# Kernel optimization log

Hardware: AMD Instinct MI355X
Metric: run time of the kernel (lower is better)

Reference implementation:

```python
import jax, jax.numpy as jnp
import numpy as np

N_NODES = 100000
N_EDGES = 1600000


def gcn_conv(x, edge_index, W, b):
    """PyG-style GCNConv: self-loops + symmetric normalization + scatter-add."""
    n = x.shape[0]
    src, dst = edge_index[0], edge_index[1]
    loop = jnp.arange(n, dtype=src.dtype)
    src = jnp.concatenate([src, loop])
    dst = jnp.concatenate([dst, loop])
    h = x @ W  # [n, out] transform before propagate (PyG order)
    deg = jax.ops.segment_sum(jnp.ones_like(dst, dtype=h.dtype), dst, num_segments=n)
    dinv = jnp.where(deg > 0, deg ** -0.5, 0.0)
    norm = dinv[src] * dinv[dst]  # [E+n]
    msgs = h[src] * norm[:, None]  # gather + scale (largest intermediate)
    out = jax.ops.segment_sum(msgs, dst, num_segments=n)
    return out + b


def setup_inputs() -> dict:
    key = jax.random.key(0)
    ks = jax.random.split(key, 8)
    edge_attr = jax.random.normal(ks[0], (N_NODES, 5), dtype=jnp.float32)
    edge_index = jax.random.randint(ks[1], (2, N_EDGES), 0, N_NODES, dtype=jnp.int64)
    def lin(k, fan_in, fan_out):
        bound = 1.0 / np.sqrt(fan_in)
        return jax.random.uniform(k, (fan_in, fan_out), jnp.float32, -bound, bound)
    return {
        "edge_attr": edge_attr,
        "edge_index": edge_index,
        "W1": lin(ks[2], 5, 64),
        "b1": jnp.zeros((64,), jnp.float32),
        "W2": lin(ks[3], 64, 32),
        "b2": jnp.zeros((32,), jnp.float32),
        "fcW1": lin(ks[4], 32, 16),
        "fcb1": jnp.zeros((16,), jnp.float32),
        "fcW2": lin(ks[5], 16, 2),
        "fcb2": jnp.zeros((2,), jnp.float32),
    }


def reference(edge_attr, edge_index, W1, b1, W2, b2, fcW1, fcb1, fcW2, fcb2):
    x = jax.nn.relu(gcn_conv(edge_attr, edge_index, W1, b1))
    x = jax.nn.relu(gcn_conv(x, edge_index, W2, b2))
    x = jax.nn.relu(x @ fcW1 + fcb1)
    return x @ fcW2 + fcb2
```

## Files before the change

### kernel.cpp

```cpp
#include <hip/hip_runtime.h>


#define MS_TILE 2048
#define MAXB 512
#define AGG_NODES 32
#define AGG_STAGE 1024

__global__ __launch_bounds__(256) void histA(const int* __restrict__ dst,
                                             int* __restrict__ histG, int E) {
    __shared__ int h[MAXB];
    int t = threadIdx.x;
    h[t] = 0;
    h[t + 256] = 0;
    __syncthreads();
    int base = blockIdx.x * MS_TILE;
    int cnt = min(MS_TILE, E - base);
    for (int k = t; k < cnt; k += 256) atomicAdd(&h[dst[base + k] >> 8], 1);
    __syncthreads();
    histG[blockIdx.x * MAXB + t] = h[t];
    histG[blockIdx.x * MAXB + 256 + t] = h[t + 256];
}

__global__ __launch_bounds__(256) void scanTiles(const int* __restrict__ histG,
                                                 int* __restrict__ offsG,
                                                 int* __restrict__ bucketTotal,
                                                 int nTiles) {
    __shared__ int scn[256];
    int b = blockIdx.x, t = threadIdx.x;
    int run = 0;
    for (int base = 0; base < nTiles; base += 256) {
        int idx = base + t;
        int v = (idx < nTiles) ? histG[idx * MAXB + b] : 0;
        scn[t] = v;
        __syncthreads();
        int incl = v;
        for (int d = 1; d < 256; d <<= 1) {
            int add = (t >= d) ? scn[t - d] : 0;
            __syncthreads();
            incl += add;
            scn[t] = incl;
            __syncthreads();
        }
        if (idx < nTiles) offsG[idx * MAXB + b] = incl - v + run;
        run += scn[255];
        __syncthreads();
    }
    if (t == 0) bucketTotal[b] = run;
}

__global__ __launch_bounds__(256) void scanBase(const int* __restrict__ bucketTotal,
                                                int* __restrict__ gbase, int E) {
    __shared__ int scn[256];
    int t = threadIdx.x;
    int a0 = bucketTotal[2 * t], a1 = bucketTotal[2 * t + 1];
    int s = a0 + a1;
    scn[t] = s;
    __syncthreads();
    int incl = s;
    for (int d = 1; d < 256; d <<= 1) {
        int add = (t >= d) ? scn[t - d] : 0;
        __syncthreads();
        incl += add;
        scn[t] = incl;
        __syncthreads();
    }
    int ex = incl - s;
    gbase[2 * t] = ex;
    gbase[2 * t + 1] = ex + a0;
    if (t == 255) gbase[MAXB] = E;
}

__global__ __launch_bounds__(256) void multisplit2(
    const int* __restrict__ src, const int* __restrict__ dst,
    const int* __restrict__ histG, const int* __restrict__ offsG,
    const int* __restrict__ gbase, unsigned* __restrict__ binned, int E) {
    __shared__ unsigned stage[MS_TILE];
    __shared__ unsigned short sb[MS_TILE];
    __shared__ int hoff[MAXB + 1];
    __shared__ int hcur[MAXB];
    __shared__ int gb[MAXB];
    __shared__ int scn[256];
    int t = threadIdx.x;
    int tile = blockIdx.x;
    int base = tile * MS_TILE;
    int cnt = min(MS_TILE, E - base);

    int a0 = histG[tile * MAXB + 2 * t];
    int a1 = histG[tile * MAXB + 2 * t + 1];
    gb[2 * t] = gbase[2 * t] + offsG[tile * MAXB + 2 * t];
    gb[2 * t + 1] = gbase[2 * t + 1] + offsG[tile * MAXB + 2 * t + 1];
    int s = a0 + a1;
    scn[t] = s;
    __syncthreads();
    int incl = s;
    for (int d = 1; d < 256; d <<= 1) {
        int add = (t >= d) ? scn[t - d] : 0;
        __syncthreads();
        incl += add;
        scn[t] = incl;
        __syncthreads();
    }
    int ex = incl - s;
    hoff[2 * t] = ex;
    hoff[2 * t + 1] = ex + a0;
    hcur[2 * t] = ex;
    hcur[2 * t + 1] = ex + a0;
    if (t == 255) hoff[MAXB] = cnt;
    __syncthreads();
    for (int k = t; k < cnt; k += 256) {
        int d = dst[base + k];
        int b = d >> 8;
        int p = atomicAdd(&hcur[b], 1);
        stage[p] = ((unsigned)src[base + k] << 8) | (unsigned)(d & 255);
        sb[p] = (unsigned short)b;
    }
    __syncthreads();
    for (int k = t; k < cnt; k += 256) {
        int b = sb[k];
        binned[gb[b] + (k - hoff[b])] = stage[k];
    }
}

__global__ __launch_bounds__(256) void place_fine2(
    const unsigned* __restrict__ binned, const int* __restrict__ gbase,
    const float* __restrict__ x, int* __restrict__ offs, int* __restrict__ deg,
    float* __restrict__ dinv, float* __restrict__ y, int* __restrict__ srcs, int n) {
    __shared__ int cnt[256];
    __shared__ int scn[256];
    __shared__ int lcur[256];
    int t = threadIdx.x, b = blockIdx.x;
    int node0 = b << 8;
    int nn = min(256, n - node0);
    int e0 = gbase[b], e1 = gbase[b + 1];
    cnt[t] = 0;
    __syncthreads();
    for (int k = e0 + t; k < e1; k += 256) atomicAdd(&cnt[binned[k] & 255u], 1);
    __syncthreads();
    int c = cnt[t];
    scn[t] = c;
    __syncthreads();
    int incl = c;
    for (int d = 1; d < 256; d <<= 1) {
        int add = (t >= d) ? scn[t - d] : 0;
        __syncthreads();
        incl += add;
        scn[t] = incl;
        __syncthreads();
    }
    int myoff = e0 + (incl - c);
    lcur[t] = myoff;
    if (t < nn) {
        int node = node0 + t;
        offs[node] = myoff;
        deg[node] = c;
        float di = 1.0f / sqrtf((float)(c + 1));
        dinv[node] = di;
        const float* xr = x + (size_t)node * 5;
        float4 a = {xr[0] * di, xr[1] * di, xr[2] * di, xr[3] * di};
        float4 bq = {xr[4] * di, 0.f, 0.f, 0.f};
        *(float4*)(y + (size_t)node * 8) = a;
        *(float4*)(y + (size_t)node * 8 + 4) = bq;
    }
    __syncthreads();
    for (int k = e0 + t; k < e1; k += 256) {
        unsigned w = binned[k];
        int p = atomicAdd(&lcur[w & 255u], 1);
        srcs[p] = (int)(w >> 8);
    }
}

__global__ void agg_xin(const float* __restrict__ y, const int* __restrict__ srcs,
                        const int* __restrict__ offs, const int* __restrict__ deg,
                        const float* __restrict__ dinv, float* __restrict__ z, int n) {
    int i = blockIdx.x * blockDim.x + threadIdx.x;
    if (i >= n) return;
    const float4* yv = (const float4*)y;
    float4 a = yv[(size_t)i * 2];
    float4 b = yv[(size_t)i * 2 + 1];
    int off = offs[i], cnt = deg[i];
    int p = 0;
    for (; p + 2 <= cnt; p += 2) {
        int s0 = srcs[off + p], s1 = srcs[off + p + 1];
        float4 v0 = yv[(size_t)s0 * 2];
        float4 w0 = yv[(size_t)s0 * 2 + 1];
        float4 v1 = yv[(size_t)s1 * 2];
        float4 w1 = yv[(size_t)s1 * 2 + 1];
        a.x += v0.x + v1.x; a.y += v0.y + v1.y; a.z += v0.z + v1.z; a.w += v0.w + v1.w;
        b.x += w0.x + w1.x;
    }
    if (p < cnt) {
        int s0 = srcs[off + p];
        float4 v0 = yv[(size_t)s0 * 2];
        float w0 = y[(size_t)s0 * 8 + 4];
        a.x += v0.x; a.y += v0.y; a.z += v0.z; a.w += v0.w;
        b.x += w0;
    }
    float di = dinv[i];
    float4 oa = {a.x * di, a.y * di, a.z * di, a.w * di};
    float4 ob = {b.x * di, 0.f, 0.f, 0.f};
    float4* zv = (float4*)z;
    zv[(size_t)i * 2] = oa;
    zv[(size_t)i * 2 + 1] = ob;
}

__global__ __launch_bounds__(256) void transform12(
    const float* __restrict__ z, const float* __restrict__ W1,
    const float* __restrict__ b1, const float* __restrict__ W2,
    const float* __restrict__ dinv, float* __restrict__ h2, int n) {
    __shared__ float w1s[320];
    __shared__ float b1s[64];
    __shared__ float w2s[64 * 32];
    __shared__ float o1[32 * 64];
    int t = threadIdx.x;
    w1s[t] = W1[t];
    if (t < 64) {
        w1s[t + 256] = W1[t + 256];
        b1s[t] = b1[t];
    }
#pragma unroll
    for (int r = 0; r < 8; ++r) w2s[r * 256 + t] = W2[r * 256 + t];
    __syncthreads();
    int node0 = blockIdx.x * 32;
#pragma unroll
    for (int r = 0; r < 8; ++r) {
        int idx = r * 256 + t;
        int li = idx >> 6, f = idx & 63;
        int i = node0 + li;
        if (i < n) {
            const float* zr = z + (size_t)i * 8;
            float acc = b1s[f];
#pragma unroll
            for (int k = 0; k < 5; ++k) acc += zr[k] * w1s[k * 64 + f];
            o1[li * 64 + f] = fmaxf(acc, 0.0f);
        }
    }
    __syncthreads();
#pragma unroll
    for (int r = 0; r < 4; ++r) {
        int idx = r * 256 + t;
        int li = idx >> 5, g = idx & 31;
        int i = node0 + li;
        if (i < n) {
            float acc = 0.f;
#pragma unroll
            for (int k = 0; k < 64; ++k) acc += o1[li * 64 + k] * w2s[k * 32 + g];
            h2[(size_t)i * 32 + g] = acc * dinv[i];
        }
    }
}

__global__ __launch_bounds__(256) void agg2_fc(
    const float* __restrict__ h, const int* __restrict__ srcs,
    const int* __restrict__ offs, const int* __restrict__ deg,
    const float* __restrict__ dinv, const float* __restrict__ b2,
    const float* __restrict__ fcW1, const float* __restrict__ fcb1,
    const float* __restrict__ fcW2, const float* __restrict__ fcb2,
    float* __restrict__ out, int n, int E) {
    __shared__ int sidx[AGG_STAGE];
    __shared__ float sm[AGG_NODES * 33];
    __shared__ float x3s[AGG_NODES * 16];
    __shared__ float w1s[512];
    __shared__ float w2s[32];
    __shared__ float b1s[16];
    __shared__ float b2s[2];
    __shared__ float bs2[32];
    int t = threadIdx.x;
    w1s[t] = fcW1[t];
    w1s[t + 256] = fcW1[t + 256];
    if (t < 32) { w2s[t] = fcW2[t]; bs2[t] = b2[t]; }
    if (t < 16) b1s[t] = fcb1[t];
    if (t < 2) b2s[t] = fcb2[t];

    int node0 = blockIdx.x * AGG_NODES;
    int li = t >> 3, fq = t & 7;
    int i = node0 + li;
    bool live = (i < n);
    const char* hb = (const char*)h;

    int e0 = offs[node0];
    int eEnd = (node0 + AGG_NODES < n) ? offs[node0 + AGG_NODES] : E;
    int myOff = 0, myCnt = 0;
    float4 acc = {0.f, 0.f, 0.f, 0.f};
    if (live) {
        myOff = offs[i];
        myCnt = deg[i];
        acc = *(const float4*)(hb + ((size_t)i << 7) + (fq << 4));
    }

    for (int cs = e0; cs < eEnd; cs += AGG_STAGE) {
        int ce = min(cs + AGG_STAGE, eEnd);
        for (int k = cs + t; k < ce; k += 256) sidx[k - cs] = srcs[k] << 7;
        __syncthreads();
        int ps = max(myOff, cs), pe = min(myOff + myCnt, ce);
        int p = ps;
        for (; p + 4 <= pe; p += 4) {
            int o0 = sidx[p - cs];
            int o1 = sidx[p + 1 - cs];
            int o2 = sidx[p + 2 - cs];
            int o3 = sidx[p + 3 - cs];
            float4 v0 = *(const float4*)(hb + o0 + (fq << 4));
            float4 v1 = *(const float4*)(hb + o1 + (fq << 4));
            float4 v2 = *(const float4*)(hb + o2 + (fq << 4));
            float4 v3 = *(const float4*)(hb + o3 + (fq << 4));
            acc.x += (v0.x + v1.x) + (v2.x + v3.x);
            acc.y += (v0.y + v1.y) + (v2.y + v3.y);
            acc.z += (v0.z + v1.z) + (v2.z + v3.z);
            acc.w += (v0.w + v1.w) + (v2.w + v3.w);
        }
        for (; p < pe; ++p) {
            float4 v = *(const float4*)(hb + sidx[p - cs] + (fq << 4));
            acc.x += v.x; acc.y += v.y; acc.z += v.z; acc.w += v.w;
        }
        __syncthreads();
    }

    if (live) {
        float di = dinv[i];
        int f0 = fq << 2;
        sm[li * 33 + f0 + 0] = fmaxf(di * acc.x + bs2[f0 + 0], 0.f);
        sm[li * 33 + f0 + 1] = fmaxf(di * acc.y + bs2[f0 + 1], 0.f);
        sm[li * 33 + f0 + 2] = fmaxf(di * acc.z + bs2[f0 + 2], 0.f);
        sm[li * 33 + f0 + 3] = fmaxf(di * acc.w + bs2[f0 + 3], 0.f);
    }
    __syncthreads();
#pragma unroll
    for (int r = 0; r < 2; ++r) {
        int idx = r * 256 + t;
        int lj = idx >> 4, j = idx & 15;
        if (node0 + lj < n) {
            float a = b1s[j];
#pragma unroll
            for (int k = 0; k < 32; ++k) a += sm[lj * 33 + k] * w1s[k * 16 + j];
            x3s[lj * 16 + j] = fmaxf(a, 0.f);
        }
    }
    __syncthreads();
    if (t < 64) {
        int lj = t >> 1, o = t & 1;
        if (node0 + lj < n) {
            float a = b2s[o];
#pragma unroll
            for (int j = 0; j < 16; ++j) a += x3s[lj * 16 + j] * w2s[j * 2 + o];
            out[(size_t)(node0 + lj) * 2 + o] = a;
        }
    }
}

extern "C" void kernel_launch(void* const* d_in, const int* in_sizes, int n_in,
                              void* d_out, int out_size, void* d_ws, size_t ws_size,
                              hipStream_t stream) {
    const float* edge_attr = (const float*)d_in[0];
    const int* edge_index  = (const int*)d_in[1];
    const float* W1   = (const float*)d_in[2];
    const float* b1   = (const float*)d_in[3];
    const float* W2   = (const float*)d_in[4];
    const float* b2   = (const float*)d_in[5];
    const float* fcW1 = (const float*)d_in[6];
    const float* fcb1 = (const float*)d_in[7];
    const float* fcW2 = (const float*)d_in[8];
    const float* fcb2 = (const float*)d_in[9];
    float* out = (float*)d_out;

    int n = in_sizes[0] / 5;
    int E = in_sizes[1] / 2;
    int NBkt = (n + 255) >> 8;
    int nTiles = (E + MS_TILE - 1) / MS_TILE;
    const int* src = edge_index;
    const int* dst = edge_index + E;

    char* ws = (char*)d_ws;
    auto alloc = [&](size_t bytes) {
        char* p = ws;
        ws += (bytes + 255) & ~(size_t)255;
        return p;
    };
    int*      deg    = (int*)alloc((size_t)n * 4);
    int*      offs   = (int*)alloc((size_t)n * 4);
    float*    dinv   = (float*)alloc((size_t)n * 4);
    int*      histG  = (int*)alloc((size_t)nTiles * MAXB * 4);
    int*      offsG  = (int*)alloc((size_t)nTiles * MAXB * 4);
    int*      btot   = (int*)alloc((size_t)MAXB * 4);
    int*      gbase  = (int*)alloc((size_t)(MAXB + 1) * 4);
    int*      srcs   = (int*)alloc((size_t)E * 4);
    unsigned* binned = (unsigned*)alloc((size_t)E * 4);
    float*    y      = (float*)alloc((size_t)n * 8 * 4);
    float*    z      = (float*)alloc((size_t)n * 8 * 4);
    float*    h2     = (float*)alloc((size_t)n * 32 * 4);

    histA<<<nTiles, 256, 0, stream>>>(dst, histG, E);
    scanTiles<<<MAXB, 256, 0, stream>>>(histG, offsG, btot, nTiles);
    scanBase<<<1, 256, 0, stream>>>(btot, gbase, E);
    multisplit2<<<nTiles, 256, 0, stream>>>(src, dst, histG, offsG, gbase, binned, E);
    place_fine2<<<NBkt, 256, 0, stream>>>(binned, gbase, edge_attr, offs, deg, dinv,
                                          y, srcs, n);

    agg_xin<<<(n + 255) / 256, 256, 0, stream>>>(y, srcs, offs, deg, dinv, z, n);
    transform12<<<(n + 31) / 32, 256, 0, stream>>>(z, W1, b1, W2, dinv, h2, n);
    agg2_fc<<<(n + AGG_NODES - 1) / AGG_NODES, 256, 0, stream>>>(
        h2, srcs, offs, deg, dinv, b2, fcW1, fcb1, fcW2, fcb2, out, n, E);
}
```

Before: 200.0 us.

## Fuse scanBase into multisplit and layer-1 aggregation into transform kernel

Removes the single-block scanBase launch by having every multisplit2 block redundantly scan the 512 bucket totals, with tile 0 writing gbase for later kernels. Merges agg_xin and transform12 into one kernel that keeps aggregated features in shared memory, dropping the z round-trip through global memory and one launch. Adds an 8-wide unrolled gather in agg2_fc for more loads in flight. In exchange, every multisplit block does an extra scan, and the fused kernel uses more shared memory with 256-node blocks, which may lower occupancy.

```diff
diff --git a/kernel.cpp b/kernel.cpp
--- a/kernel.cpp
+++ b/kernel.cpp
@@ -48,32 +48,11 @@
     if (t == 0) bucketTotal[b] = run;
 }
 
-__global__ __launch_bounds__(256) void scanBase(const int* __restrict__ bucketTotal,
-                                                int* __restrict__ gbase, int E) {
-    __shared__ int scn[256];
-    int t = threadIdx.x;
-    int a0 = bucketTotal[2 * t], a1 = bucketTotal[2 * t + 1];
-    int s = a0 + a1;
-    scn[t] = s;
-    __syncthreads();
-    int incl = s;
-    for (int d = 1; d < 256; d <<= 1) {
-        int add = (t >= d) ? scn[t - d] : 0;
-        __syncthreads();
-        incl += add;
-        scn[t] = incl;
-        __syncthreads();
-    }
-    int ex = incl - s;
-    gbase[2 * t] = ex;
-    gbase[2 * t + 1] = ex + a0;
-    if (t == 255) gbase[MAXB] = E;
-}
-
 __global__ __launch_bounds__(256) void multisplit2(
     const int* __restrict__ src, const int* __restrict__ dst,
     const int* __restrict__ histG, const int* __restrict__ offsG,
-    const int* __restrict__ gbase, unsigned* __restrict__ binned, int E) {
+    const int* __restrict__ btot, int* __restrict__ gbaseOut,
+    unsigned* __restrict__ binned, int E) {
     __shared__ unsigned stage[MS_TILE];
     __shared__ unsigned short sb[MS_TILE];
     __shared__ int hoff[MAXB + 1];
@@ -85,10 +64,29 @@
     int base = tile * MS_TILE;
     int cnt = min(MS_TILE, E - base);
 
+    int b0 = btot[2 * t], b1v = btot[2 * t + 1];
+    int s2 = b0 + b1v;
+    scn[t] = s2;
+    __syncthreads();
+    int incl2 = s2;
+    for (int d = 1; d < 256; d <<= 1) {
+        int add = (t >= d) ? scn[t - d] : 0;
+        __syncthreads();
+        incl2 += add;
+        scn[t] = incl2;
+        __syncthreads();
+    }
+    int ex2 = incl2 - s2;
+    gb[2 * t] = ex2 + offsG[tile * MAXB + 2 * t];
+    gb[2 * t + 1] = ex2 + b0 + offsG[tile * MAXB + 2 * t + 1];
+    if (tile == 0) {
+        gbaseOut[2 * t] = ex2;
+        gbaseOut[2 * t + 1] = ex2 + b0;
+        if (t == 255) gbaseOut[MAXB] = E;
+    }
+
     int a0 = histG[tile * MAXB + 2 * t];
     int a1 = histG[tile * MAXB + 2 * t + 1];
-    gb[2 * t] = gbase[2 * t] + offsG[tile * MAXB + 2 * t];
-    gb[2 * t + 1] = gbase[2 * t + 1] + offsG[tile * MAXB + 2 * t + 1];
     int s = a0 + a1;
     scn[t] = s;
     __syncthreads();
@@ -169,44 +167,13 @@
     }
 }
 
-__global__ void agg_xin(const float* __restrict__ y, const int* __restrict__ srcs,
-                        const int* __restrict__ offs, const int* __restrict__ deg,
-                        const float* __restrict__ dinv, float* __restrict__ z, int n) {
-    int i = blockIdx.x * blockDim.x + threadIdx.x;
-    if (i >= n) return;
-    const float4* yv = (const float4*)y;
-    float4 a = yv[(size_t)i * 2];
-    float4 b = yv[(size_t)i * 2 + 1];
-    int off = offs[i], cnt = deg[i];
-    int p = 0;
-    for (; p + 2 <= cnt; p += 2) {
-        int s0 = srcs[off + p], s1 = srcs[off + p + 1];
-        float4 v0 = yv[(size_t)s0 * 2];
-        float4 w0 = yv[(size_t)s0 * 2 + 1];
-        float4 v1 = yv[(size_t)s1 * 2];
-        float4 w1 = yv[(size_t)s1 * 2 + 1];
-        a.x += v0.x + v1.x; a.y += v0.y + v1.y; a.z += v0.z + v1.z; a.w += v0.w + v1.w;
-        b.x += w0.x + w1.x;
-    }
-    if (p < cnt) {
-        int s0 = srcs[off + p];
-        float4 v0 = yv[(size_t)s0 * 2];
-        float w0 = y[(size_t)s0 * 8 + 4];
-        a.x += v0.x; a.y += v0.y; a.z += v0.z; a.w += v0.w;
-        b.x += w0;
-    }
-    float di = dinv[i];
-    float4 oa = {a.x * di, a.y * di, a.z * di, a.w * di};
-    float4 ob = {b.x * di, 0.f, 0.f, 0.f};
-    float4* zv = (float4*)z;
-    zv[(size_t)i * 2] = oa;
-    zv[(size_t)i * 2 + 1] = ob;
-}
-
-__global__ __launch_bounds__(256) void transform12(
-    const float* __restrict__ z, const float* __restrict__ W1,
+__global__ __launch_bounds__(256) void agg1_transform(
+    const float* __restrict__ y, const int* __restrict__ srcs,
+    const int* __restrict__ offs, const int* __restrict__ deg,
+    const float* __restrict__ dinv, const float* __restrict__ W1,
     const float* __restrict__ b1, const float* __restrict__ W2,
-    const float* __restrict__ dinv, float* __restrict__ h2, int n) {
+    float* __restrict__ h2, int n) {
+    __shared__ float zs[256 * 9];
     __shared__ float w1s[320];
     __shared__ float b1s[64];
     __shared__ float w2s[64 * 32];
@@ -219,33 +186,70 @@
     }
 #pragma unroll
     for (int r = 0; r < 8; ++r) w2s[r * 256 + t] = W2[r * 256 + t];
-    __syncthreads();
-    int node0 = blockIdx.x * 32;
-#pragma unroll
-    for (int r = 0; r < 8; ++r) {
-        int idx = r * 256 + t;
-        int li = idx >> 6, f = idx & 63;
-        int i = node0 + li;
-        if (i < n) {
-            const float* zr = z + (size_t)i * 8;
-            float acc = b1s[f];
-#pragma unroll
-            for (int k = 0; k < 5; ++k) acc += zr[k] * w1s[k * 64 + f];
-            o1[li * 64 + f] = fmaxf(acc, 0.0f);
-        }
-    }
-    __syncthreads();
-#pragma unroll
-    for (int r = 0; r < 4; ++r) {
-        int idx = r * 256 + t;
-        int li = idx >> 5, g = idx & 31;
-        int i = node0 + li;
-        if (i < n) {
-            float acc = 0.f;
-#pragma unroll
-            for (int k = 0; k < 64; ++k) acc += o1[li * 64 + k] * w2s[k * 32 + g];
-            h2[(size_t)i * 32 + g] = acc * dinv[i];
-        }
+
+    int node0 = blockIdx.x * 256;
+    int i = node0 + t;
+    if (i < n) {
+        const float4* yv = (const float4*)y;
+        float4 a = yv[(size_t)i * 2];
+        float4 b = yv[(size_t)i * 2 + 1];
+        int off = offs[i], cnt = deg[i];
+        int p = 0;
+        for (; p + 2 <= cnt; p += 2) {
+            int s0 = srcs[off + p], s1 = srcs[off + p + 1];
+            float4 v0 = yv[(size_t)s0 * 2];
+            float4 w0 = yv[(size_t)s0 * 2 + 1];
+            float4 v1 = yv[(size_t)s1 * 2];
+            float4 w1 = yv[(size_t)s1 * 2 + 1];
+            a.x += v0.x + v1.x; a.y += v0.y + v1.y;
+            a.z += v0.z + v1.z; a.w += v0.w + v1.w;
+            b.x += w0.x + w1.x;
+        }
+        if (p < cnt) {
+            int s0 = srcs[off + p];
+            float4 v0 = yv[(size_t)s0 * 2];
+            float w0 = y[(size_t)s0 * 8 + 4];
+            a.x += v0.x; a.y += v0.y; a.z += v0.z; a.w += v0.w;
+            b.x += w0;
+        }
+        float di = dinv[i];
+        zs[t * 9 + 0] = a.x * di;
+        zs[t * 9 + 1] = a.y * di;
+        zs[t * 9 + 2] = a.z * di;
+        zs[t * 9 + 3] = a.w * di;
+        zs[t * 9 + 4] = b.x * di;
+        zs[t * 9 + 8] = di;
+    }
+    __syncthreads();
+#pragma unroll
+    for (int c = 0; c < 8; ++c) {
+        int cbase = c * 32;
+#pragma unroll
+        for (int r = 0; r < 8; ++r) {
+            int idx = r * 256 + t;
+            int li = idx >> 6, f = idx & 63;
+            if (node0 + cbase + li < n) {
+                const float* zr = zs + (cbase + li) * 9;
+                float acc = b1s[f];
+#pragma unroll
+                for (int k = 0; k < 5; ++k) acc += zr[k] * w1s[k * 64 + f];
+                o1[li * 64 + f] = fmaxf(acc, 0.0f);
+            }
+        }
+        __syncthreads();
+#pragma unroll
+        for (int r = 0; r < 4; ++r) {
+            int idx = r * 256 + t;
+            int li = idx >> 5, g = idx & 31;
+            int i2 = node0 + cbase + li;
+            if (i2 < n) {
+                float acc = 0.f;
+#pragma unroll
+                for (int k = 0; k < 64; ++k) acc += o1[li * 64 + k] * w2s[k * 32 + g];
+                h2[(size_t)i2 * 32 + g] = acc * zs[(cbase + li) * 9 + 8];
+            }
+        }
+        __syncthreads();
     }
 }
 
@@ -293,11 +297,23 @@
         __syncthreads();
         int ps = max(myOff, cs), pe = min(myOff + myCnt, ce);
         int p = ps;
+        for (; p + 8 <= pe; p += 8) {
+            int o[8];
+#pragma unroll
+            for (int u = 0; u < 8; ++u) o[u] = sidx[p + u - cs];
+            float4 v[8];
+#pragma unroll
+            for (int u = 0; u < 8; ++u)
+                v[u] = *(const float4*)(hb + o[u] + (fq << 4));
+#pragma unroll
+            for (int u = 0; u < 8; ++u) {
+                acc.x += v[u].x; acc.y += v[u].y;
+                acc.z += v[u].z; acc.w += v[u].w;
+            }
+        }
         for (; p + 4 <= pe; p += 4) {
-            int o0 = sidx[p - cs];
-            int o1 = sidx[p + 1 - cs];
-            int o2 = sidx[p + 2 - cs];
-            int o3 = sidx[p + 3 - cs];
+            int o0 = sidx[p - cs], o1 = sidx[p + 1 - cs];
+            int o2 = sidx[p + 2 - cs], o3 = sidx[p + 3 - cs];
             float4 v0 = *(const float4*)(hb + o0 + (fq << 4));
             float4 v1 = *(const float4*)(hb + o1 + (fq << 4));
             float4 v2 = *(const float4*)(hb + o2 + (fq << 4));
@@ -384,18 +400,16 @@
     int*      srcs   = (int*)alloc((size_t)E * 4);
     unsigned* binned = (unsigned*)alloc((size_t)E * 4);
     float*    y      = (float*)alloc((size_t)n * 8 * 4);
-    float*    z      = (float*)alloc((size_t)n * 8 * 4);
     float*    h2     = (float*)alloc((size_t)n * 32 * 4);
 
     histA<<<nTiles, 256, 0, stream>>>(dst, histG, E);
     scanTiles<<<MAXB, 256, 0, stream>>>(histG, offsG, btot, nTiles);
-    scanBase<<<1, 256, 0, stream>>>(btot, gbase, E);
-    multisplit2<<<nTiles, 256, 0, stream>>>(src, dst, histG, offsG, gbase, binned, E);
+    multisplit2<<<nTiles, 256, 0, stream>>>(src, dst, histG, offsG, btot, gbase,
+                                            binned, E);
     place_fine2<<<NBkt, 256, 0, stream>>>(binned, gbase, edge_attr, offs, deg, dinv,
                                           y, srcs, n);
-
-    agg_xin<<<(n + 255) / 256, 256, 0, stream>>>(y, srcs, offs, deg, dinv, z, n);
-    transform12<<<(n + 31) / 32, 256, 0, stream>>>(z, W1, b1, W2, dinv, h2, n);
+    agg1_transform<<<(n + 255) / 256, 256, 0, stream>>>(y, srcs, offs, deg, dinv,
+                                                        W1, b1, W2, h2, n);
     agg2_fc<<<(n + AGG_NODES - 1) / AGG_NODES, 256, 0, stream>>>(
         h2, srcs, offs, deg, dinv, b2, fcW1, fcb1, fcW2, fcb2, out, n, E);
 }
```

Result: no change. 203.1 us (+1.5%).
